# Performance work log

Measured on AMD Instinct MI355X. Metric: run time of the kernel, lower is better.

## Reference

```python
import jax, jax.numpy as jnp
import numpy as np

TOKEN_DIM = 256
NUM_HEADS = 2
IN_DIMS = 512
D = TOKEN_DIM * NUM_HEADS  # 512
SCALE = TOKEN_DIM ** (-0.5)


def _l2norm(v, axis):
    # torch F.normalize: v / max(||v||_2, eps)
    n = jnp.sqrt(jnp.sum(v * v, axis=axis, keepdims=True))
    return v / jnp.maximum(n, 1e-12)


def setup_inputs() -> dict:
    key = jax.random.key(0)
    ks = jax.random.split(key, 10)
    b, n = 8, 4096
    x = jax.random.normal(ks[0], (b, n, IN_DIMS), dtype=jnp.float32)
    s = 0.02
    Wq = jax.random.normal(ks[1], (IN_DIMS, D), dtype=jnp.float32) * s
    bq = jax.random.normal(ks[2], (D,), dtype=jnp.float32) * s
    Wk = jax.random.normal(ks[3], (IN_DIMS, D), dtype=jnp.float32) * s
    bk = jax.random.normal(ks[4], (D,), dtype=jnp.float32) * s
    Wr = jax.random.normal(ks[5], (D, TOKEN_DIM), dtype=jnp.float32) * s
    br = jax.random.normal(ks[6], (TOKEN_DIM,), dtype=jnp.float32) * s
    w_alpha = jax.random.normal(ks[7], (D, 1), dtype=jnp.float32)
    w_beta = jax.random.normal(ks[8], (D, 1), dtype=jnp.float32)
    return {"x": x, "Wq": Wq, "bq": bq, "Wk": Wk, "bk": bk,
            "Wr": Wr, "br": br, "w_alpha": w_alpha, "w_beta": w_beta}


def reference(x, Wq, bq, Wk, bk, Wr, br, w_alpha, w_beta):
    # x: [b, n, in_dims]
    q = x @ Wq + bq                      # [b, n, D]
    k = x @ Wk + bk                      # [b, n, D]
    q = _l2norm(q, axis=-1)
    k = _l2norm(k, axis=-1)
    v = _l2norm(k, axis=-1)              # original bug: value = normalize(key)

    alpha_w = (q @ w_alpha) * SCALE      # [b, n, 1]
    alpha_w = _l2norm(alpha_w, axis=1)   # normalize over token axis
    g_q = jnp.sum(alpha_w * q, axis=1)   # [b, D]
    g_q = jax.nn.softmax(g_q, axis=-1)

    p = g_q[:, None, :] * k              # [b, n, D]
    beta_w = _l2norm((p @ w_beta) * SCALE, axis=1)  # [b, n, 1]
    g_k = jnp.sum(beta_w * p, axis=1)    # [b, D]
    g_k = jax.nn.softmax(g_k, axis=-1)

    kvi = g_k[:, None, :] * v + q        # [b, n, D]
    return kvi @ Wr + br                 # [b, n, token_dim]
```

## Files before the change

kernel.cpp:

```cpp
#include <hip/hip_runtime.h>
#include <hip/hip_bf16.h>
#include <stdint.h>

#define BATCH    8
#define NTOKB    4096
#define NTOK     (BATCH * NTOKB)
#define DIN      512
#define DD       512
#define TD       256
#define SCALE    0.0625f
#define LSTR     36

typedef unsigned short ushortT;
typedef __attribute__((ext_vector_type(8))) short  short8;
typedef __attribute__((ext_vector_type(4))) float  f32x4;

union Frag { uint4 u; short8 s; };

__device__ __forceinline__ float bf_lo(uint32_t u) { return __uint_as_float(u << 16); }
__device__ __forceinline__ float bf_hi(uint32_t u) { return __uint_as_float(u & 0xffff0000u); }
__device__ __forceinline__ ushortT f2bf(float f) {
    uint32_t u = __float_as_uint(f);
    return (ushortT)((u + 0x7fffu + ((u >> 16) & 1u)) >> 16);
}
__device__ __forceinline__ short8 lds_frag(const ushortT* p) {
    uint2 a = *reinterpret_cast<const uint2*>(p);
    uint2 b = *reinterpret_cast<const uint2*>(p + 4);
    Frag f; f.u.x = a.x; f.u.y = a.y; f.u.z = b.x; f.u.w = b.y;
    return f.s;
}
__device__ __forceinline__ void gload_lds16(const ushortT* g, ushortT* l) {
    __builtin_amdgcn_global_load_lds(
        (const __attribute__((address_space(1))) uint32_t*)(const void*)g,
        (__attribute__((address_space(3))) uint32_t*)(void*)l,
        16, 0, 0);
}

__global__ __launch_bounds__(256) void packw_kernel(
    const float* __restrict__ Wq, const float* __restrict__ Wk,
    const float* __restrict__ Wr, ushortT* __restrict__ W16)
{
    const int blk = blockIdx.x;
    if (blk < 32) {
        const int mat = blk >> 4, c = blk & 15;
        const float* S = mat ? Wk : Wq;
        ushortT* D = W16 + (size_t)mat * (512 * 512) + (size_t)c * 16384;
        for (int i = threadIdx.x; i < 16384; i += 256) {
            int n = i & 511, p = i >> 9;
            int l = ((p >> 3) ^ ((n >> 1) & 3)) * 8 + (p & 7);
            D[n * 32 + p] = f2bf(S[(size_t)(c * 32 + l) * 512 + n]);
        }
    } else {
        const int c = blk - 32;
        ushortT* D = W16 + (size_t)2 * (512 * 512) + (size_t)c * 8192;
        for (int i = threadIdx.x; i < 8192; i += 256) {
            int n = i & 255, p = i >> 8;
            int l = ((p >> 3) ^ ((n >> 1) & 3)) * 8 + (p & 7);
            D[n * 32 + p] = f2bf(Wr[(size_t)(c * 32 + l) * 256 + n]);
        }
    }
}

__global__ __launch_bounds__(512) void gemm_qk_kernel(
    const float* __restrict__ x, const ushortT* __restrict__ W16,
    const float* __restrict__ bq, const float* __restrict__ bk,
    const float* __restrict__ w_alpha,
    ushortT* __restrict__ qn, ushortT* __restrict__ kn,
    float* __restrict__ alpha_raw)
{
    __shared__ __align__(16) ushortT xs[64 * LSTR];
    __shared__ __align__(16) ushortT wsd[512 * 32];
    __shared__ float rowsq[8][64];
    __shared__ float alphap[8][64];
    __shared__ float rnorm_s[64];

    const int tid = threadIdx.x;
    const size_t tok0 = (size_t)blockIdx.x * 64;

    const int lane = tid & 63, w = tid >> 6;
    const int m = lane & 15, quad = lane >> 4;

    const int xtok = tid >> 3;
    const int xkg  = (tid & 7) * 4;
    const float* xsrc = x + (tok0 + xtok) * DIN;

    for (int mat = 0; mat < 2; ++mat) {
        const ushortT* Wb = W16 + (size_t)mat * (512 * 512);
        const float* bias = mat ? bk : bq;
        ushortT* dst = mat ? kn : qn;

        f32x4 acc[4][4];
        #pragma unroll
        for (int tr = 0; tr < 4; ++tr)
            #pragma unroll
            for (int tc = 0; tc < 4; ++tc) acc[tr][tc] = (f32x4){0.f, 0.f, 0.f, 0.f};

        for (int c = 0; c < 16; ++c) {
            __syncthreads();
            {
                float4 xv = *reinterpret_cast<const float4*>(xsrc + c * 32 + xkg);
                ushort4 xb;
                xb.x = f2bf(xv.x); xb.y = f2bf(xv.y); xb.z = f2bf(xv.z); xb.w = f2bf(xv.w);
                *reinterpret_cast<ushort4*>(&xs[xtok * LSTR + xkg]) = xb;
            }
            {
                const ushortT* wsrc = Wb + (size_t)c * 16384;
                #pragma unroll
                for (int i = 0; i < 4; ++i) {
                    const int region = i * 8 + w;
                    gload_lds16(wsrc + region * 512 + lane * 8, &wsd[region * 512]);
                }
            }
            __syncthreads();
            {
                short8 af[4], bfv[4];
                #pragma unroll
                for (int tr = 0; tr < 4; ++tr)
                    af[tr] = lds_frag(&xs[(tr * 16 + m) * LSTR + quad * 8]);
                #pragma unroll
                for (int tc = 0; tc < 4; ++tc) {
                    const int n = w * 64 + tc * 16 + m;
                    bfv[tc] = *reinterpret_cast<const short8*>(
                        &wsd[n * 32 + ((quad ^ ((n >> 1) & 3)) * 8)]);
                }
                #pragma unroll
                for (int tr = 0; tr < 4; ++tr)
                    #pragma unroll
                    for (int tc = 0; tc < 4; ++tc)
                        acc[tr][tc] = __builtin_amdgcn_mfma_f32_16x16x32_bf16(af[tr], bfv[tc], acc[tr][tc], 0, 0, 0);
            }
        }

        float biasv[4], wa[4];
        #pragma unroll
        for (int tc = 0; tc < 4; ++tc) {
            biasv[tc] = bias[w * 64 + tc * 16 + m];
            wa[tc] = (mat == 0) ? w_alpha[w * 64 + tc * 16 + m] : 0.f;
        }
        #pragma unroll
        for (int tr = 0; tr < 4; ++tr)
            #pragma unroll
            for (int tc = 0; tc < 4; ++tc)
                #pragma unroll
                for (int reg = 0; reg < 4; ++reg)
                    acc[tr][tc][reg] += biasv[tc];

        __syncthreads();
        #pragma unroll
        for (int tr = 0; tr < 4; ++tr) {
            #pragma unroll
            for (int reg = 0; reg < 4; ++reg) {
                float s = 0.f, a = 0.f;
                #pragma unroll
                for (int tc = 0; tc < 4; ++tc) {
                    float v = acc[tr][tc][reg];
                    s = fmaf(v, v, s);
                    a = fmaf(v, wa[tc], a);
                }
                #pragma unroll
                for (int off = 1; off < 16; off <<= 1) {
                    s += __shfl_xor(s, off);
                    a += __shfl_xor(a, off);
                }
                if (m == 0) {
                    rowsq[w][tr * 16 + quad * 4 + reg] = s;
                    alphap[w][tr * 16 + quad * 4 + reg] = a;
                }
            }
        }
        __syncthreads();
        if (tid < 64) {
            float ss = 0.f, aa = 0.f;
            #pragma unroll
            for (int w2 = 0; w2 < 8; ++w2) { ss += rowsq[w2][tid]; aa += alphap[w2][tid]; }
            float rn = 1.0f / fmaxf(sqrtf(ss), 1e-12f);
            rnorm_s[tid] = rn;
            if (mat == 0) alpha_raw[tok0 + tid] = SCALE * aa * rn;
        }
        __syncthreads();
        #pragma unroll
        for (int tr = 0; tr < 4; ++tr) {
            #pragma unroll
            for (int reg = 0; reg < 4; ++reg) {
                float rn = rnorm_s[tr * 16 + quad * 4 + reg];
                size_t row = tok0 + tr * 16 + quad * 4 + reg;
                ushortT* rp = dst + row * DD + w * 64 + m;
                #pragma unroll
                for (int tc = 0; tc < 4; ++tc)
                    rp[tc * 16] = f2bf(acc[tr][tc][reg] * rn);
            }
        }
    }
}

__global__ __launch_bounds__(256) void norm_kernel(const float* __restrict__ in,
                                                   float* __restrict__ inv_out)
{
    int b = blockIdx.x;
    __shared__ float red[256];
    float s = 0.f;
    for (int i = threadIdx.x; i < NTOKB; i += 256) {
        float v = in[b * NTOKB + i];
        s = fmaf(v, v, s);
    }
    red[threadIdx.x] = s;
    __syncthreads();
    for (int off = 128; off > 0; off >>= 1) {
        if (threadIdx.x < off) red[threadIdx.x] += red[threadIdx.x + off];
        __syncthreads();
    }
    if (threadIdx.x == 0) inv_out[b] = 1.0f / fmaxf(sqrtf(red[0]), 1e-12f);
}

__global__ __launch_bounds__(256) void wsum_kernel(const ushortT* __restrict__ M,
                                                   const float* __restrict__ raw,
                                                   const float* __restrict__ invp,
                                                   float* __restrict__ dst)
{
    const int blk = blockIdx.x, tid = threadIdx.x;
    const int b = blk >> 6;
    const int i0 = (blk & 63) * 64;
    __shared__ float wr[64];
    if (tid < 64) wr[tid] = raw[(size_t)b * NTOKB + i0 + tid];
    __syncthreads();
    const uint32_t* M32 = reinterpret_cast<const uint32_t*>(M);
    size_t base = ((size_t)b * NTOKB + i0) * 256 + tid;
    float a0 = 0.f, a1 = 0.f;
    for (int ii = 0; ii < 64; ++ii) {
        uint32_t v = M32[base + (size_t)ii * 256];
        float wv = wr[ii];
        a0 = fmaf(wv, bf_lo(v), a0);
        a1 = fmaf(wv, bf_hi(v), a1);
    }
    float iv = invp[b];
    atomicAdd(&dst[b * DD + 2 * tid],     a0 * iv);
    atomicAdd(&dst[b * DD + 2 * tid + 1], a1 * iv);
}

__global__ __launch_bounds__(256) void softmax_kernel(const float* __restrict__ in,
                                                      const float* __restrict__ mul,
                                                      const float* __restrict__ wbeta,
                                                      float* __restrict__ out,
                                                      float* __restrict__ wb2)
{
    int b = blockIdx.x, tid = threadIdx.x;
    __shared__ float red[256];
    float v0 = in[b * DD + tid], v1 = in[b * DD + 256 + tid];
    if (mul) { v0 *= mul[b * DD + tid]; v1 *= mul[b * DD + 256 + tid]; }
    red[tid] = fmaxf(v0, v1);
    __syncthreads();
    for (int off = 128; off > 0; off >>= 1) {
        if (tid < off) red[tid] = fmaxf(red[tid], red[tid + off]);
        __syncthreads();
    }
    float m = red[0];
    __syncthreads();
    float e0 = expf(v0 - m), e1 = expf(v1 - m);
    red[tid] = e0 + e1;
    __syncthreads();
    for (int off = 128; off > 0; off >>= 1) {
        if (tid < off) red[tid] += red[tid + off];
        __syncthreads();
    }
    float rs = 1.0f / red[0];
    float o0 = e0 * rs, o1 = e1 * rs;
    out[b * DD + tid] = o0;
    out[b * DD + 256 + tid] = o1;
    if (wb2) {
        wb2[b * DD + tid]       = o0 * wbeta[tid];
        wb2[b * DD + 256 + tid] = o1 * wbeta[256 + tid];
    }
}

__global__ __launch_bounds__(256) void beta_kernel(const ushortT* __restrict__ kn,
                                                   const float* __restrict__ wb2,
                                                   float* __restrict__ beta_raw)
{
    int wave = threadIdx.x >> 6, lane = threadIdx.x & 63;
    size_t tok = (size_t)blockIdx.x * 4 + wave;
    int b = (int)(tok >> 12);
    uint4 kv = *reinterpret_cast<const uint4*>(kn + tok * DD + lane * 8);
    float4 wv0 = *reinterpret_cast<const float4*>(wb2 + b * DD + lane * 8);
    float4 wv1 = *reinterpret_cast<const float4*>(wb2 + b * DD + lane * 8 + 4);
    float s = bf_lo(kv.x) * wv0.x + bf_hi(kv.x) * wv0.y
            + bf_lo(kv.y) * wv0.z + bf_hi(kv.y) * wv0.w
            + bf_lo(kv.z) * wv1.x + bf_hi(kv.z) * wv1.y
            + bf_lo(kv.w) * wv1.z + bf_hi(kv.w) * wv1.w;
    #pragma unroll
    for (int off = 32; off > 0; off >>= 1) s += __shfl_xor(s, off);
    if (lane == 0) beta_raw[tok] = SCALE * s;
}

__global__ __launch_bounds__(256) void out_mfma_kernel(
    const ushortT* __restrict__ qn, const ushortT* __restrict__ kn,
    const float* __restrict__ g_k, const ushortT* __restrict__ WrT,
    const float* __restrict__ br, float* __restrict__ out)
{
    __shared__ __align__(16) ushortT kvs[64 * LSTR];
    __shared__ __align__(16) ushortT wrs[256 * 32];
    __shared__ float gks[512];

    const int tid = threadIdx.x;
    const size_t tok0 = (size_t)blockIdx.x * 64;
    const int b = (int)(tok0 >> 12);

    gks[tid] = g_k[b * DD + tid];
    gks[256 + tid] = g_k[b * DD + 256 + tid];

    const int lane = tid & 63, w = tid >> 6;
    const int m = lane & 15, quad = lane >> 4;

    f32x4 acc[4][4];
    #pragma unroll
    for (int tr = 0; tr < 4; ++tr)
        #pragma unroll
        for (int tc = 0; tc < 4; ++tc) acc[tr][tc] = (f32x4){0.f, 0.f, 0.f, 0.f};

    const int st  = tid >> 2;
    const int skg = (tid & 3) * 8;

    for (int c = 0; c < 16; ++c) {
        __syncthreads();
        {
            const size_t base = (tok0 + st) * DD + c * 32 + skg;
            uint4 qv = *reinterpret_cast<const uint4*>(qn + base);
            uint4 kv = *reinterpret_cast<const uint4*>(kn + base);
            const float* g = &gks[c * 32 + skg];
            ushortT o[8];
            o[0] = f2bf(fmaf(g[0], bf_lo(kv.x), bf_lo(qv.x)));
            o[1] = f2bf(fmaf(g[1], bf_hi(kv.x), bf_hi(qv.x)));
            o[2] = f2bf(fmaf(g[2], bf_lo(kv.y), bf_lo(qv.y)));
            o[3] = f2bf(fmaf(g[3], bf_hi(kv.y), bf_hi(qv.y)));
            o[4] = f2bf(fmaf(g[4], bf_lo(kv.z), bf_lo(qv.z)));
            o[5] = f2bf(fmaf(g[5], bf_hi(kv.z), bf_hi(qv.z)));
            o[6] = f2bf(fmaf(g[6], bf_lo(kv.w), bf_lo(qv.w)));
            o[7] = f2bf(fmaf(g[7], bf_hi(kv.w), bf_hi(qv.w)));
            uint2* lp = reinterpret_cast<uint2*>(&kvs[st * LSTR + skg]);
            lp[0] = make_uint2(((uint32_t)o[1] << 16) | o[0], ((uint32_t)o[3] << 16) | o[2]);
            lp[1] = make_uint2(((uint32_t)o[5] << 16) | o[4], ((uint32_t)o[7] << 16) | o[6]);
        }
        {
            const ushortT* wsrc = WrT + (size_t)c * 8192;
            #pragma unroll
            for (int i = 0; i < 4; ++i) {
                const int region = i * 4 + w;
                gload_lds16(wsrc + region * 512 + lane * 8, &wrs[region * 512]);
            }
        }
        __syncthreads();
        {
            short8 af[4], bfr[4];
            #pragma unroll
            for (int tr = 0; tr < 4; ++tr)
                af[tr] = lds_frag(&kvs[(tr * 16 + m) * LSTR + quad * 8]);
            #pragma unroll
            for (int tc = 0; tc < 4; ++tc) {
                const int n = w * 64 + tc * 16 + m;
                bfr[tc] = *reinterpret_cast<const short8*>(
                    &wrs[n * 32 + ((quad ^ ((n >> 1) & 3)) * 8)]);
            }
            #pragma unroll
            for (int tr = 0; tr < 4; ++tr)
                #pragma unroll
                for (int tc = 0; tc < 4; ++tc)
                    acc[tr][tc] = __builtin_amdgcn_mfma_f32_16x16x32_bf16(af[tr], bfr[tc], acc[tr][tc], 0, 0, 0);
        }
    }

    float brv[4];
    #pragma unroll
    for (int tc = 0; tc < 4; ++tc) brv[tc] = br[w * 64 + tc * 16 + m];
    #pragma unroll
    for (int tr = 0; tr < 4; ++tr) {
        #pragma unroll
        for (int reg = 0; reg < 4; ++reg) {
            size_t row = tok0 + tr * 16 + quad * 4 + reg;
            float* rp = out + row * TD + w * 64 + m;
            #pragma unroll
            for (int tc = 0; tc < 4; ++tc)
                rp[tc * 16] = acc[tr][tc][reg] + brv[tc];
        }
    }
}

extern "C" void kernel_launch(void* const* d_in, const int* in_sizes, int n_in,
                              void* d_out, int out_size, void* d_ws, size_t ws_size,
                              hipStream_t stream)
{
    const float* x       = (const float*)d_in[0];
    const float* Wq      = (const float*)d_in[1];
    const float* bq      = (const float*)d_in[2];
    const float* Wk      = (const float*)d_in[3];
    const float* bk      = (const float*)d_in[4];
    const float* Wr      = (const float*)d_in[5];
    const float* br      = (const float*)d_in[6];
    const float* w_alpha = (const float*)d_in[7];
    const float* w_beta  = (const float*)d_in[8];
    float* out = (float*)d_out;

    ushortT* kn = (ushortT*)d_out;

    char* ws = (char*)d_ws;
    ushortT* qn = (ushortT*)ws;        ws += (size_t)NTOK * DD * sizeof(ushortT);
    ushortT* W16 = (ushortT*)ws;       ws += (size_t)2 * 512 * 512 * sizeof(ushortT)
                                           + (size_t)512 * 256 * sizeof(ushortT);
    float* alpha_raw = (float*)ws;     ws += (size_t)NTOK * sizeof(float);
    float* beta_raw  = (float*)ws;     ws += (size_t)NTOK * sizeof(float);
    float* gq_raw = (float*)ws;        ws += (size_t)BATCH * DD * sizeof(float);
    float* h_raw  = (float*)ws;        ws += (size_t)BATCH * DD * sizeof(float);
    float* g_q    = (float*)ws;        ws += (size_t)BATCH * DD * sizeof(float);
    float* wb2    = (float*)ws;        ws += (size_t)BATCH * DD * sizeof(float);
    float* g_k    = (float*)ws;        ws += (size_t)BATCH * DD * sizeof(float);
    float* inv_a  = (float*)ws;        ws += 64;
    float* inv_b  = (float*)ws;        ws += 64;
    ushortT* WrT = W16 + (size_t)2 * 512 * 512;

    hipMemsetAsync(gq_raw, 0, 2 * BATCH * DD * sizeof(float), stream);

    packw_kernel<<<48, 256, 0, stream>>>(Wq, Wk, Wr, W16);
    gemm_qk_kernel<<<NTOK / 64, 512, 0, stream>>>(x, W16, bq, bk, w_alpha, qn, kn, alpha_raw);
    norm_kernel<<<BATCH, 256, 0, stream>>>(alpha_raw, inv_a);
    wsum_kernel<<<512, 256, 0, stream>>>(qn, alpha_raw, inv_a, gq_raw);
    softmax_kernel<<<BATCH, 256, 0, stream>>>(gq_raw, nullptr, w_beta, g_q, wb2);
    beta_kernel<<<NTOK / 4, 256, 0, stream>>>(kn, wb2, beta_raw);
    norm_kernel<<<BATCH, 256, 0, stream>>>(beta_raw, inv_b);
    wsum_kernel<<<512, 256, 0, stream>>>(kn, beta_raw, inv_b, h_raw);
    softmax_kernel<<<BATCH, 256, 0, stream>>>(h_raw, g_q, nullptr, g_k, nullptr);
    out_mfma_kernel<<<NTOK / 64, 256, 0, stream>>>(qn, kn, g_k, WrT, br, out);
}
```

Before: 279.0 us.

## Split Q/K GEMM across grid, fuse alpha-weighted sum and beta stages

The Q/K projection GEMM now runs Q and K as separate blocks via a second grid dimension, doubling parallelism, and the Q blocks accumulate the alpha-weighted token sum directly into gq_raw with atomics. This removes the separate wsum pass over qn. The token-axis L2 norm is deferred into the softmax kernels by scaling the raw sums there, which drops the norm kernels. Beta computation and the k-weighted sum are merged into one kernel that reads each kn tile while it is likely still cached. The cost is more global atomics and fewer kernel launches overall.

```diff
diff --git a/kernel.cpp b/kernel.cpp
--- a/kernel.cpp
+++ b/kernel.cpp
@@ -66,186 +66,172 @@
     const float* __restrict__ bq, const float* __restrict__ bk,
     const float* __restrict__ w_alpha,
     ushortT* __restrict__ qn, ushortT* __restrict__ kn,
-    float* __restrict__ alpha_raw)
+    float* __restrict__ alpha_raw, float* __restrict__ gq_raw)
 {
     __shared__ __align__(16) ushortT xs[64 * LSTR];
     __shared__ __align__(16) ushortT wsd[512 * 32];
     __shared__ float rowsq[8][64];
     __shared__ float alphap[8][64];
     __shared__ float rnorm_s[64];
+    __shared__ float alpha_sh[64];
 
     const int tid = threadIdx.x;
+    const int mat = blockIdx.y;
     const size_t tok0 = (size_t)blockIdx.x * 64;
+    const int b = (int)(blockIdx.x >> 6);
+    const ushortT* Wb = W16 + (size_t)mat * (512 * 512);
+    const float* bias = mat ? bk : bq;
+    ushortT* dst = mat ? kn : qn;
 
     const int lane = tid & 63, w = tid >> 6;
     const int m = lane & 15, quad = lane >> 4;
+
+    f32x4 acc[4][4];
+    #pragma unroll
+    for (int tr = 0; tr < 4; ++tr)
+        #pragma unroll
+        for (int tc = 0; tc < 4; ++tc) acc[tr][tc] = (f32x4){0.f, 0.f, 0.f, 0.f};
 
     const int xtok = tid >> 3;
     const int xkg  = (tid & 7) * 4;
     const float* xsrc = x + (tok0 + xtok) * DIN;
 
-    for (int mat = 0; mat < 2; ++mat) {
-        const ushortT* Wb = W16 + (size_t)mat * (512 * 512);
-        const float* bias = mat ? bk : bq;
-        ushortT* dst = mat ? kn : qn;
-
-        f32x4 acc[4][4];
-        #pragma unroll
-        for (int tr = 0; tr < 4; ++tr)
-            #pragma unroll
-            for (int tc = 0; tc < 4; ++tc) acc[tr][tc] = (f32x4){0.f, 0.f, 0.f, 0.f};
-
-        for (int c = 0; c < 16; ++c) {
-            __syncthreads();
-            {
-                float4 xv = *reinterpret_cast<const float4*>(xsrc + c * 32 + xkg);
-                ushort4 xb;
-                xb.x = f2bf(xv.x); xb.y = f2bf(xv.y); xb.z = f2bf(xv.z); xb.w = f2bf(xv.w);
-                *reinterpret_cast<ushort4*>(&xs[xtok * LSTR + xkg]) = xb;
-            }
-            {
-                const ushortT* wsrc = Wb + (size_t)c * 16384;
-                #pragma unroll
-                for (int i = 0; i < 4; ++i) {
-                    const int region = i * 8 + w;
-                    gload_lds16(wsrc + region * 512 + lane * 8, &wsd[region * 512]);
-                }
-            }
-            __syncthreads();
-            {
-                short8 af[4], bfv[4];
-                #pragma unroll
-                for (int tr = 0; tr < 4; ++tr)
-                    af[tr] = lds_frag(&xs[(tr * 16 + m) * LSTR + quad * 8]);
-                #pragma unroll
-                for (int tc = 0; tc < 4; ++tc) {
-                    const int n = w * 64 + tc * 16 + m;
-                    bfv[tc] = *reinterpret_cast<const short8*>(
-                        &wsd[n * 32 + ((quad ^ ((n >> 1) & 3)) * 8)]);
-                }
-                #pragma unroll
-                for (int tr = 0; tr < 4; ++tr)
-                    #pragma unroll
-                    for (int tc = 0; tc < 4; ++tc)
-                        acc[tr][tc] = __builtin_amdgcn_mfma_f32_16x16x32_bf16(af[tr], bfv[tc], acc[tr][tc], 0, 0, 0);
-            }
-        }
-
-        float biasv[4], wa[4];
-        #pragma unroll
-        for (int tc = 0; tc < 4; ++tc) {
-            biasv[tc] = bias[w * 64 + tc * 16 + m];
-            wa[tc] = (mat == 0) ? w_alpha[w * 64 + tc * 16 + m] : 0.f;
-        }
-        #pragma unroll
-        for (int tr = 0; tr < 4; ++tr)
-            #pragma unroll
-            for (int tc = 0; tc < 4; ++tc)
-                #pragma unroll
-                for (int reg = 0; reg < 4; ++reg)
-                    acc[tr][tc][reg] += biasv[tc];
-
-        __syncthreads();
-        #pragma unroll
-        for (int tr = 0; tr < 4; ++tr) {
-            #pragma unroll
-            for (int reg = 0; reg < 4; ++reg) {
-                float s = 0.f, a = 0.f;
-                #pragma unroll
-                for (int tc = 0; tc < 4; ++tc) {
-                    float v = acc[tr][tc][reg];
-                    s = fmaf(v, v, s);
-                    a = fmaf(v, wa[tc], a);
-                }
-                #pragma unroll
-                for (int off = 1; off < 16; off <<= 1) {
-                    s += __shfl_xor(s, off);
-                    a += __shfl_xor(a, off);
-                }
-                if (m == 0) {
-                    rowsq[w][tr * 16 + quad * 4 + reg] = s;
-                    alphap[w][tr * 16 + quad * 4 + reg] = a;
-                }
-            }
-        }
-        __syncthreads();
-        if (tid < 64) {
-            float ss = 0.f, aa = 0.f;
-            #pragma unroll
-            for (int w2 = 0; w2 < 8; ++w2) { ss += rowsq[w2][tid]; aa += alphap[w2][tid]; }
-            float rn = 1.0f / fmaxf(sqrtf(ss), 1e-12f);
-            rnorm_s[tid] = rn;
-            if (mat == 0) alpha_raw[tok0 + tid] = SCALE * aa * rn;
-        }
-        __syncthreads();
-        #pragma unroll
-        for (int tr = 0; tr < 4; ++tr) {
-            #pragma unroll
-            for (int reg = 0; reg < 4; ++reg) {
-                float rn = rnorm_s[tr * 16 + quad * 4 + reg];
-                size_t row = tok0 + tr * 16 + quad * 4 + reg;
-                ushortT* rp = dst + row * DD + w * 64 + m;
+    for (int c = 0; c < 16; ++c) {
+        __syncthreads();
+        {
+            float4 xv = *reinterpret_cast<const float4*>(xsrc + c * 32 + xkg);
+            ushort4 xb;
+            xb.x = f2bf(xv.x); xb.y = f2bf(xv.y); xb.z = f2bf(xv.z); xb.w = f2bf(xv.w);
+            *reinterpret_cast<ushort4*>(&xs[xtok * LSTR + xkg]) = xb;
+        }
+        {
+            const ushortT* wsrc = Wb + (size_t)c * 16384;
+            #pragma unroll
+            for (int i = 0; i < 4; ++i) {
+                const int region = i * 8 + w;
+                gload_lds16(wsrc + region * 512 + lane * 8, &wsd[region * 512]);
+            }
+        }
+        __syncthreads();
+        {
+            short8 af[4], bfv[4];
+            #pragma unroll
+            for (int tr = 0; tr < 4; ++tr)
+                af[tr] = lds_frag(&xs[(tr * 16 + m) * LSTR + quad * 8]);
+            #pragma unroll
+            for (int tc = 0; tc < 4; ++tc) {
+                const int n = w * 64 + tc * 16 + m;
+                bfv[tc] = *reinterpret_cast<const short8*>(
+                    &wsd[n * 32 + ((quad ^ ((n >> 1) & 3)) * 8)]);
+            }
+            #pragma unroll
+            for (int tr = 0; tr < 4; ++tr)
                 #pragma unroll
                 for (int tc = 0; tc < 4; ++tc)
-                    rp[tc * 16] = f2bf(acc[tr][tc][reg] * rn);
-            }
-        }
-    }
-}
-
-__global__ __launch_bounds__(256) void norm_kernel(const float* __restrict__ in,
-                                                   float* __restrict__ inv_out)
-{
-    int b = blockIdx.x;
+                    acc[tr][tc] = __builtin_amdgcn_mfma_f32_16x16x32_bf16(af[tr], bfv[tc], acc[tr][tc], 0, 0, 0);
+        }
+    }
+
+    float biasv[4], wa[4];
+    #pragma unroll
+    for (int tc = 0; tc < 4; ++tc) {
+        biasv[tc] = bias[w * 64 + tc * 16 + m];
+        wa[tc] = (mat == 0) ? w_alpha[w * 64 + tc * 16 + m] : 0.f;
+    }
+    #pragma unroll
+    for (int tr = 0; tr < 4; ++tr)
+        #pragma unroll
+        for (int tc = 0; tc < 4; ++tc)
+            #pragma unroll
+            for (int reg = 0; reg < 4; ++reg)
+                acc[tr][tc][reg] += biasv[tc];
+
+    __syncthreads();
+    #pragma unroll
+    for (int tr = 0; tr < 4; ++tr) {
+        #pragma unroll
+        for (int reg = 0; reg < 4; ++reg) {
+            float s = 0.f, a = 0.f;
+            #pragma unroll
+            for (int tc = 0; tc < 4; ++tc) {
+                float v = acc[tr][tc][reg];
+                s = fmaf(v, v, s);
+                a = fmaf(v, wa[tc], a);
+            }
+            #pragma unroll
+            for (int off = 1; off < 16; off <<= 1) {
+                s += __shfl_xor(s, off);
+                a += __shfl_xor(a, off);
+            }
+            if (m == 0) {
+                rowsq[w][tr * 16 + quad * 4 + reg] = s;
+                alphap[w][tr * 16 + quad * 4 + reg] = a;
+            }
+        }
+    }
+    __syncthreads();
+    if (tid < 64) {
+        float ss = 0.f, aa = 0.f;
+        #pragma unroll
+        for (int w2 = 0; w2 < 8; ++w2) { ss += rowsq[w2][tid]; aa += alphap[w2][tid]; }
+        float rn = 1.0f / fmaxf(sqrtf(ss), 1e-12f);
+        float av = SCALE * aa * rn;
+        rnorm_s[tid] = rn;
+        alpha_sh[tid] = av;
+        if (mat == 0) alpha_raw[tok0 + tid] = av;
+    }
+    __syncthreads();
+    float gqp[4] = {0.f, 0.f, 0.f, 0.f};
+    #pragma unroll
+    for (int tr = 0; tr < 4; ++tr) {
+        #pragma unroll
+        for (int reg = 0; reg < 4; ++reg) {
+            const int rloc = tr * 16 + quad * 4 + reg;
+            float rn = rnorm_s[rloc];
+            float av = alpha_sh[rloc];
+            size_t row = tok0 + rloc;
+            ushortT* rp = dst + row * DD + w * 64 + m;
+            #pragma unroll
+            for (int tc = 0; tc < 4; ++tc) {
+                float val = acc[tr][tc][reg] * rn;
+                rp[tc * 16] = f2bf(val);
+                gqp[tc] = fmaf(av, val, gqp[tc]);
+            }
+        }
+    }
+    if (mat == 0) {
+        #pragma unroll
+        for (int tc = 0; tc < 4; ++tc) {
+            float p = gqp[tc];
+            p += __shfl_xor(p, 16);
+            p += __shfl_xor(p, 32);
+            if (quad == 0)
+                atomicAdd(&gq_raw[b * DD + w * 64 + tc * 16 + m], p);
+        }
+    }
+}
+
+__global__ __launch_bounds__(256) void fused_softmax_kernel(
+    const float* __restrict__ nrm_in, const float* __restrict__ in,
+    const float* __restrict__ mul, const float* __restrict__ wbeta,
+    float* __restrict__ out, float* __restrict__ wb2)
+{
+    int b = blockIdx.x, tid = threadIdx.x;
     __shared__ float red[256];
     float s = 0.f;
-    for (int i = threadIdx.x; i < NTOKB; i += 256) {
-        float v = in[b * NTOKB + i];
+    for (int i = tid; i < NTOKB; i += 256) {
+        float v = nrm_in[b * NTOKB + i];
         s = fmaf(v, v, s);
     }
-    red[threadIdx.x] = s;
+    red[tid] = s;
     __syncthreads();
     for (int off = 128; off > 0; off >>= 1) {
-        if (threadIdx.x < off) red[threadIdx.x] += red[threadIdx.x + off];
-        __syncthreads();
-    }
-    if (threadIdx.x == 0) inv_out[b] = 1.0f / fmaxf(sqrtf(red[0]), 1e-12f);
-}
-
-__global__ __launch_bounds__(256) void wsum_kernel(const ushortT* __restrict__ M,
-                                                   const float* __restrict__ raw,
-                                                   const float* __restrict__ invp,
-                                                   float* __restrict__ dst)
-{
-    const int blk = blockIdx.x, tid = threadIdx.x;
-    const int b = blk >> 6;
-    const int i0 = (blk & 63) * 64;
-    __shared__ float wr[64];
-    if (tid < 64) wr[tid] = raw[(size_t)b * NTOKB + i0 + tid];
-    __syncthreads();
-    const uint32_t* M32 = reinterpret_cast<const uint32_t*>(M);
-    size_t base = ((size_t)b * NTOKB + i0) * 256 + tid;
-    float a0 = 0.f, a1 = 0.f;
-    for (int ii = 0; ii < 64; ++ii) {
-        uint32_t v = M32[base + (size_t)ii * 256];
-        float wv = wr[ii];
-        a0 = fmaf(wv, bf_lo(v), a0);
-        a1 = fmaf(wv, bf_hi(v), a1);
-    }
-    float iv = invp[b];
-    atomicAdd(&dst[b * DD + 2 * tid],     a0 * iv);
-    atomicAdd(&dst[b * DD + 2 * tid + 1], a1 * iv);
-}
-
-__global__ __launch_bounds__(256) void softmax_kernel(const float* __restrict__ in,
-                                                      const float* __restrict__ mul,
-                                                      const float* __restrict__ wbeta,
-                                                      float* __restrict__ out,
-                                                      float* __restrict__ wb2)
-{
-    int b = blockIdx.x, tid = threadIdx.x;
-    __shared__ float red[256];
-    float v0 = in[b * DD + tid], v1 = in[b * DD + 256 + tid];
+        if (tid < off) red[tid] += red[tid + off];
+        __syncthreads();
+    }
+    float inv = 1.0f / fmaxf(sqrtf(red[0]), 1e-12f);
+    __syncthreads();
+    float v0 = in[b * DD + tid] * inv, v1 = in[b * DD + 256 + tid] * inv;
     if (mul) { v0 *= mul[b * DD + tid]; v1 *= mul[b * DD + 256 + tid]; }
     red[tid] = fmaxf(v0, v1);
     __syncthreads();
@@ -272,23 +258,48 @@
     }
 }
 
-__global__ __launch_bounds__(256) void beta_kernel(const ushortT* __restrict__ kn,
-                                                   const float* __restrict__ wb2,
-                                                   float* __restrict__ beta_raw)
-{
-    int wave = threadIdx.x >> 6, lane = threadIdx.x & 63;
-    size_t tok = (size_t)blockIdx.x * 4 + wave;
-    int b = (int)(tok >> 12);
-    uint4 kv = *reinterpret_cast<const uint4*>(kn + tok * DD + lane * 8);
+__global__ __launch_bounds__(256) void betawsum_kernel(
+    const ushortT* __restrict__ kn, const float* __restrict__ wb2,
+    float* __restrict__ beta_raw, float* __restrict__ h_raw)
+{
+    const int blk = blockIdx.x, tid = threadIdx.x;
+    const int b = blk >> 6;
+    const int i0 = (blk & 63) * 64;
+    __shared__ float bs[64];
+
+    const int wave = tid >> 6, lane = tid & 63;
     float4 wv0 = *reinterpret_cast<const float4*>(wb2 + b * DD + lane * 8);
     float4 wv1 = *reinterpret_cast<const float4*>(wb2 + b * DD + lane * 8 + 4);
-    float s = bf_lo(kv.x) * wv0.x + bf_hi(kv.x) * wv0.y
-            + bf_lo(kv.y) * wv0.z + bf_hi(kv.y) * wv0.w
-            + bf_lo(kv.z) * wv1.x + bf_hi(kv.z) * wv1.y
-            + bf_lo(kv.w) * wv1.z + bf_hi(kv.w) * wv1.w;
-    #pragma unroll
-    for (int off = 32; off > 0; off >>= 1) s += __shfl_xor(s, off);
-    if (lane == 0) beta_raw[tok] = SCALE * s;
+
+    for (int it = 0; it < 16; ++it) {
+        const int t = it * 4 + wave;
+        const size_t tok = (size_t)b * NTOKB + i0 + t;
+        uint4 kv = *reinterpret_cast<const uint4*>(kn + tok * DD + lane * 8);
+        float s = bf_lo(kv.x) * wv0.x + bf_hi(kv.x) * wv0.y
+                + bf_lo(kv.y) * wv0.z + bf_hi(kv.y) * wv0.w
+                + bf_lo(kv.z) * wv1.x + bf_hi(kv.z) * wv1.y
+                + bf_lo(kv.w) * wv1.z + bf_hi(kv.w) * wv1.w;
+        #pragma unroll
+        for (int off = 32; off > 0; off >>= 1) s += __shfl_xor(s, off);
+        if (lane == 0) {
+            float bv = SCALE * s;
+            bs[t] = bv;
+            beta_raw[tok] = bv;
+        }
+    }
+    __syncthreads();
+
+    const uint32_t* M32 = reinterpret_cast<const uint32_t*>(kn);
+    size_t base = ((size_t)b * NTOKB + i0) * 256 + tid;
+    float a0 = 0.f, a1 = 0.f;
+    for (int ii = 0; ii < 64; ++ii) {
+        uint32_t v = M32[base + (size_t)ii * 256];
+        float wv = bs[ii];
+        a0 = fmaf(wv, bf_lo(v), a0);
+        a1 = fmaf(wv, bf_hi(v), a1);
+    }
+    atomicAdd(&h_raw[b * DD + 2 * tid],     a0);
+    atomicAdd(&h_raw[b * DD + 2 * tid + 1], a1);
 }
 
 __global__ __launch_bounds__(256) void out_mfma_kernel(
@@ -411,20 +422,17 @@
     float* g_q    = (float*)ws;        ws += (size_t)BATCH * DD * sizeof(float);
     float* wb2    = (float*)ws;        ws += (size_t)BATCH * DD * sizeof(float);
     float* g_k    = (float*)ws;        ws += (size_t)BATCH * DD * sizeof(float);
-    float* inv_a  = (float*)ws;        ws += 64;
-    float* inv_b  = (float*)ws;        ws += 64;
     ushortT* WrT = W16 + (size_t)2 * 512 * 512;
 
     hipMemsetAsync(gq_raw, 0, 2 * BATCH * DD * sizeof(float), stream);
 
     packw_kernel<<<48, 256, 0, stream>>>(Wq, Wk, Wr, W16);
-    gemm_qk_kernel<<<NTOK / 64, 512, 0, stream>>>(x, W16, bq, bk, w_alpha, qn, kn, alpha_raw);
-    norm_kernel<<<BATCH, 256, 0, stream>>>(alpha_raw, inv_a);
-    wsum_kernel<<<512, 256, 0, stream>>>(qn, alpha_raw, inv_a, gq_raw);
-    softmax_kernel<<<BATCH, 256, 0, stream>>>(gq_raw, nullptr, w_beta, g_q, wb2);
-    beta_kernel<<<NTOK / 4, 256, 0, stream>>>(kn, wb2, beta_raw);
-    norm_kernel<<<BATCH, 256, 0, stream>>>(beta_raw, inv_b);
-    wsum_kernel<<<512, 256, 0, stream>>>(kn, beta_raw, inv_b, h_raw);
-    softmax_kernel<<<BATCH, 256, 0, stream>>>(h_raw, g_q, nullptr, g_k, nullptr);
+    gemm_qk_kernel<<<dim3(NTOK / 64, 2), 512, 0, stream>>>(x, W16, bq, bk, w_alpha,
+                                                           qn, kn, alpha_raw, gq_raw);
+    fused_softmax_kernel<<<BATCH, 256, 0, stream>>>(alpha_raw, gq_raw, nullptr,
+                                                    w_beta, g_q, wb2);
+    betawsum_kernel<<<NTOK / 64, 256, 0, stream>>>(kn, wb2, beta_raw, h_raw);
+    fused_softmax_kernel<<<BATCH, 256, 0, stream>>>(beta_raw, h_raw, g_q,
+                                                    nullptr, g_k, nullptr);
     out_mfma_kernel<<<NTOK / 64, 256, 0, stream>>>(qn, kn, g_k, WrT, br, out);
 }
```

Result: faster. 232.6 us (-16.6%).
